# Performance work log

Hardware: AMD Instinct MI355X
Metric: run time of the kernel (lower is better)

Reference implementation:

```python
import jax, jax.numpy as jnp
import numpy as np

V_TH = 1.0          # HeavisideBoxcar firing threshold
SUBTHRESH = 0.5     # boxcar surrogate half-width (affects backward only)
INIT_TAU = 2.0      # membrane time constant; decay = sigmoid(init_tau)

N_IN, N_HIDDEN = 784, 1024
BATCH, STEPS = 128, 500


def setup_inputs() -> dict:
    key = jax.random.key(0)
    kx, kf, kr = jax.random.split(key, 3)
    x = jax.random.uniform(kx, (BATCH, STEPS, N_IN), dtype=jnp.float32)
    fc1 = 0.05 * jax.random.uniform(kf, (N_IN, N_HIDDEN), dtype=jnp.float32) / np.sqrt(N_IN)
    recurrent = 0.05 * jax.random.uniform(kr, (N_HIDDEN, N_HIDDEN), dtype=jnp.float32) / np.sqrt(N_HIDDEN)
    return {"x": x, "fc1": fc1, "recurrent": recurrent}


def reference(x, fc1, recurrent):
    # x: [B, T, n_in]; leaky-integrate-and-fire recurrent scan over T.
    B, T, _ = x.shape
    n_hidden = fc1.shape[1]
    n_slice = n_hidden // 10
    decay = jax.nn.sigmoid(jnp.asarray(INIT_TAU, dtype=x.dtype))

    def step(carry, x_t):
        mem, spk = carry                                   # [B, H] each
        cur = x_t @ fc1 + spk @ recurrent                  # input + recurrent current
        mem = mem * decay * (1.0 - spk) + cur              # leaky integrate with reset-by-spike
        spk = (mem >= V_TH).astype(mem.dtype)              # heaviside fire
        return (mem, spk), spk[:, :n_slice]

    init = (jnp.zeros((B, n_hidden), x.dtype), jnp.zeros((B, n_hidden), x.dtype))
    _, outs = jax.lax.scan(step, init, jnp.swapaxes(x, 0, 1))   # outs: [T, B, n_slice]
    return jnp.swapaxes(outs, 0, 1), T
```

## Files before the change

### kernel.cpp

```cpp
#include <hip/hip_runtime.h>
#include <stdint.h>

#define T_STEPS 500
#define NBATCH  128
#define NIN     784
#define KPAD    800
#define NH      1024
#define NSL     102
#define DECAY   0.8807970779778823f

typedef __attribute__((ext_vector_type(8))) short short8;
typedef __attribute__((ext_vector_type(8))) unsigned short ushort8;
typedef __attribute__((ext_vector_type(4))) float f32x4;

static __device__ __forceinline__ unsigned short f2bf(float f) {
  union { float f; unsigned u; } v; v.f = f;
  unsigned r = (v.u + 0x7FFFu + ((v.u >> 16) & 1u)) >> 16;
  return (unsigned short)r;
}
static __device__ __forceinline__ float bf2f(unsigned short s) {
  union { unsigned u; float f; } v; v.u = ((unsigned)s) << 16;
  return v.f;
}

__global__ __launch_bounds__(256) void prep_kernel(
    const float* __restrict__ fc1, unsigned short* __restrict__ fc1T,
    float* __restrict__ out_last) {
  int idx = blockIdx.x * 256 + threadIdx.x;
  if (idx < NH * KPAD) {
    int n = idx / KPAD, k = idx - n * KPAD;
    float v = (k < NIN) ? fc1[(size_t)k * NH + n] : 0.0f;
    fc1T[idx] = f2bf(v);
  }
  if (idx == 0) *out_last = 500.0f;
}

__global__ __launch_bounds__(256) void gemm_kernel(
    const float* __restrict__ x, const unsigned short* __restrict__ fc1T,
    unsigned short* __restrict__ curq) {
  __shared__ __align__(16) unsigned short Alds[128 * 40];
  __shared__ __align__(16) unsigned short Blds[128 * 40];

  const int tid = threadIdx.x;
  const int m0 = blockIdx.y * 128, n0 = blockIdx.x * 128;
  const int lane = tid & 63, wave = tid >> 6;
  const int wr = (wave >> 1) * 64, wc = (wave & 1) * 64;
  const int l16 = lane & 15, q = lane >> 4;

  const int r = tid >> 1;
  const int kofs = (tid & 1) * 16;

  f32x4 acc[4][4];
  const f32x4 zero4 = {0.0f, 0.0f, 0.0f, 0.0f};
#pragma unroll
  for (int i = 0; i < 4; ++i)
#pragma unroll
    for (int j = 0; j < 4; ++j) acc[i][j] = zero4;

  for (int k0 = 0; k0 < KPAD; k0 += 32) {
    ushort8 va0, va1;
    if (k0 + kofs < NIN) {
      const float4* src = (const float4*)(x + (size_t)(m0 + r) * NIN + k0 + kofs);
      float4 f0 = src[0], f1 = src[1], f2 = src[2], f3 = src[3];
      va0[0]=f2bf(f0.x); va0[1]=f2bf(f0.y); va0[2]=f2bf(f0.z); va0[3]=f2bf(f0.w);
      va0[4]=f2bf(f1.x); va0[5]=f2bf(f1.y); va0[6]=f2bf(f1.z); va0[7]=f2bf(f1.w);
      va1[0]=f2bf(f2.x); va1[1]=f2bf(f2.y); va1[2]=f2bf(f2.z); va1[3]=f2bf(f2.w);
      va1[4]=f2bf(f3.x); va1[5]=f2bf(f3.y); va1[6]=f2bf(f3.z); va1[7]=f2bf(f3.w);
    } else {
#pragma unroll
      for (int v = 0; v < 8; ++v) { va0[v] = 0; va1[v] = 0; }
    }
    *(ushort8*)&Alds[r * 40 + kofs]     = va0;
    *(ushort8*)&Alds[r * 40 + kofs + 8] = va1;

    const ushort8* bs = (const ushort8*)(fc1T + (size_t)(n0 + r) * KPAD + k0 + kofs);
    ushort8 vb0 = bs[0], vb1 = bs[1];
    *(ushort8*)&Blds[r * 40 + kofs]     = vb0;
    *(ushort8*)&Blds[r * 40 + kofs + 8] = vb1;

    __syncthreads();

    short8 av[4], bv[4];
#pragma unroll
    for (int i = 0; i < 4; ++i) {
      av[i] = *(const short8*)&Alds[(wr + i * 16 + l16) * 40 + q * 8];
      bv[i] = *(const short8*)&Blds[(wc + i * 16 + l16) * 40 + q * 8];
    }
#pragma unroll
    for (int i = 0; i < 4; ++i)
#pragma unroll
      for (int j = 0; j < 4; ++j)
        acc[i][j] = __builtin_amdgcn_mfma_f32_16x16x32_bf16(av[i], bv[j], acc[i][j], 0, 0, 0);

    __syncthreads();
  }

#pragma unroll
  for (int i = 0; i < 4; ++i)
#pragma unroll
    for (int j = 0; j < 4; ++j) {
      int row = m0 + wr + i * 16 + q * 4;
      int col = n0 + wc + j * 16 + l16;
#pragma unroll
      for (int rr = 0; rr < 4; ++rr)
        curq[(size_t)(row + rr) * NH + col] = f2bf(acc[i][j][rr]);
    }
}

__global__ __launch_bounds__(256) void scan_kernel(
    const unsigned short* __restrict__ curq, const float* __restrict__ wrec,
    float* __restrict__ out) {
  const int b = blockIdx.x, tid = threadIdx.x;
  const int h0 = tid * 4;

  __shared__ unsigned short lst[2][1024];
  __shared__ int cnt[2];

  unsigned lane = __builtin_amdgcn_mbcnt_hi(~0u, __builtin_amdgcn_mbcnt_lo(~0u, 0u));
  unsigned long long ltmask = (1ull << lane) - 1ull;

  float mem[4] = {0, 0, 0, 0}, rs[4] = {0, 0, 0, 0}, sp[4] = {0, 0, 0, 0};

  if (tid < 2) cnt[tid] = 0;
  __syncthreads();

  const size_t rowbase = (size_t)b * T_STEPS;

  for (int tb = 0; tb < T_STEPS; tb += 4) {
    ushort4 cv[4];
#pragma unroll
    for (int u = 0; u < 4; ++u)
      cv[u] = *(const ushort4*)&curq[(rowbase + tb + u) * NH + h0];

#pragma unroll
    for (int u = 0; u < 4; ++u) {
      const int t = tb + u;
      const int cur = t & 1, prv = cur ^ 1;
      if (tid == 0) cnt[cur] = 0;

      const int n = cnt[prv];
      for (int i = 0; i < n; ++i) {
        unsigned e = lst[prv][i];
        int j = e & 1023;
        float s = (e & 0x8000u) ? 1.0f : -1.0f;
        const float4 w = *(const float4*)&wrec[(size_t)j * NH + h0];
        rs[0] += s * w.x; rs[1] += s * w.y; rs[2] += s * w.z; rs[3] += s * w.w;
      }

      float cin[4] = {bf2f(cv[u].x), bf2f(cv[u].y), bf2f(cv[u].z), bf2f(cv[u].w)};
      float ns[4];
#pragma unroll
      for (int c = 0; c < 4; ++c) {
        float cc = cin[c] + rs[c];
        mem[c] = mem[c] * (DECAY * (1.0f - sp[c])) + cc;
        ns[c] = (mem[c] >= 1.0f) ? 1.0f : 0.0f;
      }

      if (h0 < NSL) {
        float* o = out + (rowbase + t) * NSL + h0;
        o[0] = ns[0];
        if (h0 + 1 < NSL) o[1] = ns[1];
        if (h0 + 2 < NSL) o[2] = ns[2];
        if (h0 + 3 < NSL) o[3] = ns[3];
      }

      __syncthreads();

#pragma unroll
      for (int c = 0; c < 4; ++c) {
        bool ch = (ns[c] != sp[c]);
        unsigned long long msk = __ballot(ch);
        if (msk) {
          int base = 0;
          if (lane == 0) base = atomicAdd(&cnt[cur], (int)__popcll(msk));
          base = __shfl(base, 0, 64);
          if (ch) {
            int pos = base + (int)__popcll(msk & ltmask);
            lst[cur][pos] =
                (unsigned short)((h0 + c) | (ns[c] > 0.5f ? 0x8000u : 0u));
          }
        }
        sp[c] = ns[c];
      }
      __syncthreads();
    }
  }
}

extern "C" void kernel_launch(void* const* d_in, const int* in_sizes, int n_in,
                              void* d_out, int out_size, void* d_ws, size_t ws_size,
                              hipStream_t stream) {
  const float* x    = (const float*)d_in[0];
  const float* fc1  = (const float*)d_in[1];
  const float* wrec = (const float*)d_in[2];
  float* out = (float*)d_out;

  unsigned short* fc1T = (unsigned short*)d_ws;
  unsigned short* curq = (unsigned short*)((char*)d_ws + 1638400);

  prep_kernel<<<dim3((NH * KPAD + 255) / 256), 256, 0, stream>>>(fc1, fc1T,
                                                                 out + (out_size - 1));
  gemm_kernel<<<dim3(8, 500), 256, 0, stream>>>(x, fc1T, curq);
  scan_kernel<<<dim3(NBATCH), 256, 0, stream>>>(curq, wrec, out);
}
```

Before: 778.5 us.

## Use async global-to-LDS loads in GEMM, tiled transpose, and triple-buffered scan

```diff
diff --git a/kernel.cpp b/kernel.cpp
--- a/kernel.cpp
+++ b/kernel.cpp
@@ -8,90 +8,111 @@
 #define NH      1024
 #define NSL     102
 #define DECAY   0.8807970779778823f
+#define MROWS   64000
 
 typedef __attribute__((ext_vector_type(8))) short short8;
-typedef __attribute__((ext_vector_type(8))) unsigned short ushort8;
 typedef __attribute__((ext_vector_type(4))) float f32x4;
+typedef unsigned int u32;
 
 static __device__ __forceinline__ unsigned short f2bf(float f) {
-  union { float f; unsigned u; } v; v.f = f;
-  unsigned r = (v.u + 0x7FFFu + ((v.u >> 16) & 1u)) >> 16;
+  union { float f; u32 u; } v; v.f = f;
+  u32 r = (v.u + 0x7FFFu + ((v.u >> 16) & 1u)) >> 16;
   return (unsigned short)r;
 }
 static __device__ __forceinline__ float bf2f(unsigned short s) {
-  union { unsigned u; float f; } v; v.u = ((unsigned)s) << 16;
+  union { u32 u; float f; } v; v.u = ((u32)s) << 16;
   return v.f;
+}
+static __device__ __forceinline__ u32 fu(float f) {
+  union { float f; u32 u; } v; v.f = f; return v.u;
+}
+static __device__ __forceinline__ void gl16(const void* g, void* l) {
+  __builtin_amdgcn_global_load_lds((const __attribute__((address_space(1))) u32*)g,
+                                   (__attribute__((address_space(3))) u32*)l, 16, 0, 0);
 }
 
 __global__ __launch_bounds__(256) void prep_kernel(
     const float* __restrict__ fc1, unsigned short* __restrict__ fc1T,
     float* __restrict__ out_last) {
-  int idx = blockIdx.x * 256 + threadIdx.x;
-  if (idx < NH * KPAD) {
-    int n = idx / KPAD, k = idx - n * KPAD;
-    float v = (k < NIN) ? fc1[(size_t)k * NH + n] : 0.0f;
-    fc1T[idx] = f2bf(v);
-  }
-  if (idx == 0) *out_last = 500.0f;
+  __shared__ float tile[32][33];
+  const int kb = blockIdx.x * 32, nb = blockIdx.y * 32;
+  const int tx = threadIdx.x, ty = threadIdx.y;
+#pragma unroll
+  for (int i = 0; i < 4; ++i) {
+    int k = kb + ty + i * 8, n = nb + tx;
+    tile[ty + i * 8][tx] = (k < NIN) ? fc1[(size_t)k * NH + n] : 0.0f;
+  }
+  __syncthreads();
+#pragma unroll
+  for (int i = 0; i < 4; ++i) {
+    int n = nb + ty + i * 8, k = kb + tx;
+    fc1T[(size_t)n * KPAD + k] = f2bf(tile[tx][ty + i * 8]);
+  }
+  if (kb == 0 && nb == 0 && tx == 0 && ty == 0) *out_last = 500.0f;
 }
 
 __global__ __launch_bounds__(256) void gemm_kernel(
     const float* __restrict__ x, const unsigned short* __restrict__ fc1T,
     unsigned short* __restrict__ curq) {
-  __shared__ __align__(16) unsigned short Alds[128 * 40];
-  __shared__ __align__(16) unsigned short Blds[128 * 40];
+  __shared__ __align__(16) float Af[128 * 32];
+  __shared__ __align__(16) unsigned short Bs[128 * 32];
 
   const int tid = threadIdx.x;
-  const int m0 = blockIdx.y * 128, n0 = blockIdx.x * 128;
+  const int n0 = blockIdx.x * 128, m0 = blockIdx.y * 128;
   const int lane = tid & 63, wave = tid >> 6;
   const int wr = (wave >> 1) * 64, wc = (wave & 1) * 64;
   const int l16 = lane & 15, q = lane >> 4;
 
-  const int r = tid >> 1;
-  const int kofs = (tid & 1) * 16;
+  const int a_irow = lane >> 3;
+  const int a_g = (lane & 7) ^ (a_irow & 7);
+  const int a_col = a_g * 4;
+  const int b_irow = lane >> 2;
+  const int b_col = (lane & 3) * 8;
 
   f32x4 acc[4][4];
-  const f32x4 zero4 = {0.0f, 0.0f, 0.0f, 0.0f};
+  const f32x4 z4 = {0.f, 0.f, 0.f, 0.f};
 #pragma unroll
   for (int i = 0; i < 4; ++i)
 #pragma unroll
-    for (int j = 0; j < 4; ++j) acc[i][j] = zero4;
+    for (int j = 0; j < 4; ++j) acc[i][j] = z4;
 
   for (int k0 = 0; k0 < KPAD; k0 += 32) {
-    ushort8 va0, va1;
-    if (k0 + kofs < NIN) {
-      const float4* src = (const float4*)(x + (size_t)(m0 + r) * NIN + k0 + kofs);
-      float4 f0 = src[0], f1 = src[1], f2 = src[2], f3 = src[3];
-      va0[0]=f2bf(f0.x); va0[1]=f2bf(f0.y); va0[2]=f2bf(f0.z); va0[3]=f2bf(f0.w);
-      va0[4]=f2bf(f1.x); va0[5]=f2bf(f1.y); va0[6]=f2bf(f1.z); va0[7]=f2bf(f1.w);
-      va1[0]=f2bf(f2.x); va1[1]=f2bf(f2.y); va1[2]=f2bf(f2.z); va1[3]=f2bf(f2.w);
-      va1[4]=f2bf(f3.x); va1[5]=f2bf(f3.y); va1[6]=f2bf(f3.z); va1[7]=f2bf(f3.w);
-    } else {
-#pragma unroll
-      for (int v = 0; v < 8; ++v) { va0[v] = 0; va1[v] = 0; }
-    }
-    *(ushort8*)&Alds[r * 40 + kofs]     = va0;
-    *(ushort8*)&Alds[r * 40 + kofs + 8] = va1;
-
-    const ushort8* bs = (const ushort8*)(fc1T + (size_t)(n0 + r) * KPAD + k0 + kofs);
-    ushort8 vb0 = bs[0], vb1 = bs[1];
-    *(ushort8*)&Blds[r * 40 + kofs]     = vb0;
-    *(ushort8*)&Blds[r * 40 + kofs + 8] = vb1;
-
+#pragma unroll
+    for (int l = 0; l < 4; ++l) {
+      const int rbase = wave * 32 + l * 8;
+      if (k0 + a_col < NIN)
+        gl16(x + (size_t)(m0 + rbase + a_irow) * NIN + k0 + a_col,
+             &Af[rbase * 32]);
+    }
+#pragma unroll
+    for (int l = 0; l < 2; ++l) {
+      const int rbase = wave * 32 + l * 16;
+      gl16(fc1T + (size_t)(n0 + rbase + b_irow) * KPAD + k0 + b_col,
+           &Bs[rbase * 32]);
+    }
     __syncthreads();
 
     short8 av[4], bv[4];
 #pragma unroll
     for (int i = 0; i < 4; ++i) {
-      av[i] = *(const short8*)&Alds[(wr + i * 16 + l16) * 40 + q * 8];
-      bv[i] = *(const short8*)&Blds[(wc + i * 16 + l16) * 40 + q * 8];
+      const int r = wr + i * 16 + l16;
+      const int s0 = (2 * q) ^ (l16 & 7);
+      const float4 alo = *(const float4*)&Af[r * 32 + s0 * 4];
+      const float4 ahi = *(const float4*)&Af[r * 32 + (s0 ^ 1) * 4];
+      union { short8 s; u32 u[4]; } p;
+      p.u[0] = __builtin_amdgcn_perm(fu(alo.y), fu(alo.x), 0x07060302u);
+      p.u[1] = __builtin_amdgcn_perm(fu(alo.w), fu(alo.z), 0x07060302u);
+      p.u[2] = __builtin_amdgcn_perm(fu(ahi.y), fu(ahi.x), 0x07060302u);
+      p.u[3] = __builtin_amdgcn_perm(fu(ahi.w), fu(ahi.z), 0x07060302u);
+      av[i] = p.s;
+      bv[i] = *(const short8*)&Bs[(wc + i * 16 + l16) * 32 + q * 8];
     }
 #pragma unroll
     for (int i = 0; i < 4; ++i)
 #pragma unroll
       for (int j = 0; j < 4; ++j)
-        acc[i][j] = __builtin_amdgcn_mfma_f32_16x16x32_bf16(av[i], bv[j], acc[i][j], 0, 0, 0);
-
+        acc[i][j] = __builtin_amdgcn_mfma_f32_16x16x32_bf16(av[i], bv[j],
+                                                            acc[i][j], 0, 0, 0);
     __syncthreads();
   }
 
@@ -99,8 +120,8 @@
   for (int i = 0; i < 4; ++i)
 #pragma unroll
     for (int j = 0; j < 4; ++j) {
-      int row = m0 + wr + i * 16 + q * 4;
-      int col = n0 + wc + j * 16 + l16;
+      const int row = m0 + wr + i * 16 + q * 4;
+      const int col = n0 + wc + j * 16 + l16;
 #pragma unroll
       for (int rr = 0; rr < 4; ++rr)
         curq[(size_t)(row + rr) * NH + col] = f2bf(acc[i][j][rr]);
@@ -113,69 +134,98 @@
   const int b = blockIdx.x, tid = threadIdx.x;
   const int h0 = tid * 4;
 
-  __shared__ unsigned short lst[2][1024];
-  __shared__ int cnt[2];
-
-  unsigned lane = __builtin_amdgcn_mbcnt_hi(~0u, __builtin_amdgcn_mbcnt_lo(~0u, 0u));
-  unsigned long long ltmask = (1ull << lane) - 1ull;
+  __shared__ __align__(16) unsigned short lst[3][1024];
+  __shared__ int cnt[3];
+
+  const unsigned lane =
+      __builtin_amdgcn_mbcnt_hi(~0u, __builtin_amdgcn_mbcnt_lo(~0u, 0u));
+  const unsigned long long ltmask = (1ull << lane) - 1ull;
 
   float mem[4] = {0, 0, 0, 0}, rs[4] = {0, 0, 0, 0}, sp[4] = {0, 0, 0, 0};
-
-  if (tid < 2) cnt[tid] = 0;
+  if (tid < 3) cnt[tid] = 0;
   __syncthreads();
 
   const size_t rowbase = (size_t)b * T_STEPS;
 
+  ushort4 cv[2][4];
+#pragma unroll
+  for (int u = 0; u < 4; ++u)
+    cv[0][u] = *(const ushort4*)&curq[(rowbase + u) * NH + h0];
+
   for (int tb = 0; tb < T_STEPS; tb += 4) {
-    ushort4 cv[4];
-#pragma unroll
-    for (int u = 0; u < 4; ++u)
-      cv[u] = *(const ushort4*)&curq[(rowbase + tb + u) * NH + h0];
-
+    const int cb = (tb >> 2) & 1;
+    if (tb + 4 < T_STEPS) {
+#pragma unroll
+      for (int u = 0; u < 4; ++u)
+        cv[cb ^ 1][u] = *(const ushort4*)&curq[(rowbase + tb + 4 + u) * NH + h0];
+    }
 #pragma unroll
     for (int u = 0; u < 4; ++u) {
       const int t = tb + u;
-      const int cur = t & 1, prv = cur ^ 1;
-      if (tid == 0) cnt[cur] = 0;
-
+      const int cur = t % 3, prv = (t + 2) % 3, nxt = (t + 1) % 3;
       const int n = cnt[prv];
-      for (int i = 0; i < n; ++i) {
-        unsigned e = lst[prv][i];
-        int j = e & 1023;
-        float s = (e & 0x8000u) ? 1.0f : -1.0f;
-        const float4 w = *(const float4*)&wrec[(size_t)j * NH + h0];
-        rs[0] += s * w.x; rs[1] += s * w.y; rs[2] += s * w.z; rs[3] += s * w.w;
-      }
-
-      float cin[4] = {bf2f(cv[u].x), bf2f(cv[u].y), bf2f(cv[u].z), bf2f(cv[u].w)};
-      float ns[4];
+      if (tid == 0) cnt[nxt] = 0;
+
+      float cin[4] = {bf2f(cv[cb][u].x), bf2f(cv[cb][u].y),
+                      bf2f(cv[cb][u].z), bf2f(cv[cb][u].w)};
+      float nm[4], ns[4];
 #pragma unroll
       for (int c = 0; c < 4; ++c) {
-        float cc = cin[c] + rs[c];
-        mem[c] = mem[c] * (DECAY * (1.0f - sp[c])) + cc;
-        ns[c] = (mem[c] >= 1.0f) ? 1.0f : 0.0f;
-      }
-
-      if (h0 < NSL) {
-        float* o = out + (rowbase + t) * NSL + h0;
-        o[0] = ns[0];
-        if (h0 + 1 < NSL) o[1] = ns[1];
-        if (h0 + 2 < NSL) o[2] = ns[2];
-        if (h0 + 3 < NSL) o[3] = ns[3];
-      }
-
-      __syncthreads();
+        nm[c] = mem[c] * (DECAY * (1.0f - sp[c])) + (cin[c] + rs[c]);
+        ns[c] = (nm[c] >= 1.0f) ? 1.0f : 0.0f;
+      }
+      if (__builtin_expect(n != 0, 0)) {
+        int i = 0;
+        for (; i + 8 <= n; i += 8) {
+          ushort4 ea = *(const ushort4*)&lst[prv][i];
+          ushort4 eb = *(const ushort4*)&lst[prv][i + 4];
+          const unsigned short es[8] = {ea.x, ea.y, ea.z, ea.w,
+                                        eb.x, eb.y, eb.z, eb.w};
+#pragma unroll
+          for (int e = 0; e < 8; ++e) {
+            const int j = es[e] & 1023;
+            const float s = (es[e] & 0x8000u) ? 1.0f : -1.0f;
+            const float4 w = *(const float4*)&wrec[(size_t)j * NH + h0];
+            rs[0] += s * w.x; rs[1] += s * w.y;
+            rs[2] += s * w.z; rs[3] += s * w.w;
+          }
+        }
+        for (; i < n; ++i) {
+          const unsigned e = lst[prv][i];
+          const int j = e & 1023;
+          const float s = (e & 0x8000u) ? 1.0f : -1.0f;
+          const float4 w = *(const float4*)&wrec[(size_t)j * NH + h0];
+          rs[0] += s * w.x; rs[1] += s * w.y;
+          rs[2] += s * w.z; rs[3] += s * w.w;
+        }
+#pragma unroll
+        for (int c = 0; c < 4; ++c) {
+          nm[c] = mem[c] * (DECAY * (1.0f - sp[c])) + (cin[c] + rs[c]);
+          ns[c] = (nm[c] >= 1.0f) ? 1.0f : 0.0f;
+        }
+      }
+#pragma unroll
+      for (int c = 0; c < 4; ++c) mem[c] = nm[c];
+
+      if (h0 + 4 <= NSL) {
+        float2* o = (float2*)(out + (rowbase + t) * NSL + h0);
+        o[0] = make_float2(ns[0], ns[1]);
+        o[1] = make_float2(ns[2], ns[3]);
+      } else if (h0 < NSL) {
+        float2* o = (float2*)(out + (rowbase + t) * NSL + h0);
+        o[0] = make_float2(ns[0], ns[1]);
+      }
 
 #pragma unroll
       for (int c = 0; c < 4; ++c) {
-        bool ch = (ns[c] != sp[c]);
-        unsigned long long msk = __ballot(ch);
+        const bool ch = (ns[c] != sp[c]);
+        const unsigned long long msk = __ballot(ch);
         if (msk) {
           int base = 0;
           if (lane == 0) base = atomicAdd(&cnt[cur], (int)__popcll(msk));
           base = __shfl(base, 0, 64);
           if (ch) {
-            int pos = base + (int)__popcll(msk & ltmask);
+            const int pos = base + (int)__popcll(msk & ltmask);
             lst[cur][pos] =
                 (unsigned short)((h0 + c) | (ns[c] > 0.5f ? 0x8000u : 0u));
           }
@@ -198,8 +248,8 @@
   unsigned short* fc1T = (unsigned short*)d_ws;
   unsigned short* curq = (unsigned short*)((char*)d_ws + 1638400);
 
-  prep_kernel<<<dim3((NH * KPAD + 255) / 256), 256, 0, stream>>>(fc1, fc1T,
-                                                                 out + (out_size - 1));
+  prep_kernel<<<dim3(25, 32), dim3(32, 8), 0, stream>>>(fc1, fc1T,
+                                                        out + (out_size - 1));
   gemm_kernel<<<dim3(8, 500), 256, 0, stream>>>(x, fc1T, curq);
   scan_kernel<<<dim3(NBATCH), 256, 0, stream>>>(curq, wrec, out);
 }
```

New measurement: 810.8 us. 1.04x slower.
